# Kernel optimization log

Hardware: AMD Instinct MI355X
Metric: run time of the kernel (lower is better)

## Reference

```python
import jax, jax.numpy as jnp
from jax import lax
import numpy as np

B, C, H, W = 4, 128, 256, 256
HEADS = 8
MID = 256


def conv2d(x, w, stride=1, pad=0, groups=1, mode='zeros'):
    if pad:
        m = 'reflect' if mode == 'reflect' else 'constant'
        x = jnp.pad(x, ((0, 0), (0, 0), (pad, pad), (pad, pad)), mode=m)
    return lax.conv_general_dilated(
        x, w, (stride, stride), 'VALID',
        dimension_numbers=('NCHW', 'OIHW', 'NCHW'),
        feature_group_count=groups)


def layernorm(x, w, b, eps=1e-5):
    # torch LayerNorm over channel dim (applied to b (hw) c layout)
    mu = jnp.mean(x, axis=1, keepdims=True)
    var = jnp.mean((x - mu) ** 2, axis=1, keepdims=True)
    xn = (x - mu) * lax.rsqrt(var + eps)
    return xn * w[None, :, None, None] + b[None, :, None, None]


def l2norm(x, eps=1e-12):
    n = jnp.sqrt(jnp.sum(x * x, axis=-1, keepdims=True))
    return x / jnp.maximum(n, eps)


def setup_inputs() -> dict:
    key = jax.random.key(0)
    ks = jax.random.split(key, 20)
    s = 0.02
    inp = {
        'x': jax.random.normal(ks[0], (B, C, H, W), jnp.float32),
        'illu_feat': jax.random.uniform(ks[1], (B, C, H, W), jnp.float32),
        'ln1_w': jnp.ones((C,), jnp.float32),
        'ln1_b': jnp.zeros((C,), jnp.float32),
        'q_w': jax.random.normal(ks[2], (C, 1, 3, 3), jnp.float32) * s,
        'k_w': jax.random.normal(ks[3], (C, C, 3, 3), jnp.float32) * s,
        'v_w': jax.random.normal(ks[4], (C, C, 1, 1), jnp.float32) * s,
        'a1_w': jax.random.normal(ks[5], (C, 1, 3, 3), jnp.float32) * s,
        'a2_w': jax.random.normal(ks[6], (C // 2, C, 1, 1), jnp.float32) * s,
        'a2_b': jnp.zeros((C // 2,), jnp.float32),
        'temp_a': jnp.ones((HEADS, 1, 1), jnp.float32),
        'temp_v': jnp.ones((HEADS, 1, 1), jnp.float32),
        'po_w': jax.random.normal(ks[7], (C, C, 1, 1), jnp.float32) * s,
        'ln2_w': jnp.ones((C,), jnp.float32),
        'ln2_b': jnp.zeros((C,), jnp.float32),
        'p1_w': jax.random.normal(ks[8], (MID, C, 1, 1), jnp.float32) * s,
        'p1_b': jnp.zeros((MID,), jnp.float32),
        'dw_w': jax.random.normal(ks[9], (MID, 1, 3, 3), jnp.float32) * s,
        'dw_b': jnp.zeros((MID,), jnp.float32),
        'p2_w': jax.random.normal(ks[10], (C, MID, 1, 1), jnp.float32) * s,
        'p2_b': jnp.zeros((C,), jnp.float32),
    }
    return inp


def reference(x, illu_feat, ln1_w, ln1_b, q_w, k_w, v_w, a1_w, a2_w, a2_b,
              temp_a, temp_v, po_w, ln2_w, ln2_b, p1_w, p1_b, dw_w, dw_b,
              p2_w, p2_b):
    b, c, h, w = x.shape
    # ---- Attention branch ----
    xn = layernorm(x, ln1_w, ln1_b)
    q = conv2d(xn, q_w, stride=2, pad=1, groups=c, mode='reflect')  # (b,c,h/2,w/2)
    k = conv2d(xn, k_w, stride=2, pad=1, mode='reflect')            # (b,c,h/2,w/2)
    v = conv2d(xn, v_w) * illu_feat                                 # (b,c,h,w)
    a = conv2d(conv2d(xn, a1_w, stride=2, pad=1, groups=c, mode='reflect'), a2_w)
    a = a + a2_b[None, :, None, None]                               # (b,c/2,h/2,w/2)

    h2, w2 = q.shape[-2:]
    l4 = h2 * w2
    cp = c // HEADS            # channels per head (q,k,v)
    ca = (c // 2) // HEADS     # channels per head (a)
    qr = l2norm(q.reshape(b, HEADS, cp, l4))
    kr = l2norm(k.reshape(b, HEADS, cp, l4))
    ar = l2norm(a.reshape(b, HEADS, ca, l4))
    vr = v.reshape(b, HEADS, cp, h * w)

    attn_a = jax.nn.softmax(jnp.einsum('bhcl,bhdl->bhcd', qr, ar) * temp_a, axis=-1)
    attn_k = jax.nn.softmax(jnp.einsum('bhdl,bhcl->bhdc', ar, kr) * temp_v, axis=-1)
    out_v = jnp.einsum('bhdc,bhcm->bhdm', attn_k, vr)   # (b,h,ca,HW)
    out = jnp.einsum('bhcd,bhdm->bhcm', attn_a, out_v)  # (b,h,cp,HW)
    out = out.reshape(b, c, h, w)
    x = x + conv2d(out, po_w)

    # ---- FFN branch ----
    y = layernorm(x, ln2_w, ln2_b)
    y = conv2d(y, p1_w) + p1_b[None, :, None, None]
    y = conv2d(y, dw_w, pad=1, groups=MID) + dw_b[None, :, None, None]
    y = jax.nn.relu(y)
    y = conv2d(y, p2_w) + p2_b[None, :, None, None]
    return x + y
```

## Files before the change

kernel.cpp:

```cpp
#include <hip/hip_runtime.h>

#define BB 4
#define CC 128
#define HH 256
#define WW 256
#define HWSZ 65536
#define H2 128
#define W2 128
#define L4SZ 16384
#define MIDC 256
#define NHEADS 8

typedef __attribute__((ext_vector_type(8))) short short8;
typedef __attribute__((ext_vector_type(4))) short s16x4;
typedef __attribute__((ext_vector_type(4))) float f32x4;
typedef __attribute__((ext_vector_type(4))) unsigned u32x4;
typedef __attribute__((ext_vector_type(2))) unsigned u32x2;

__device__ __forceinline__ short f2bf(float v) {
  unsigned u = __builtin_bit_cast(unsigned, v);
  u += 0x7fffu + ((u >> 16) & 1u);
  return (short)(u >> 16);
}
__device__ __forceinline__ unsigned pk2(float a, float b) {
  return (unsigned)(unsigned short)f2bf(a) | ((unsigned)(unsigned short)f2bf(b) << 16);
}
__device__ __forceinline__ float bflo(unsigned u) { return __builtin_bit_cast(float, u << 16); }
__device__ __forceinline__ float bfhi(unsigned u) { return __builtin_bit_cast(float, u & 0xffff0000u); }
__device__ __forceinline__ float b2f(short s) {
  return __builtin_bit_cast(float, ((unsigned)(unsigned short)s) << 16);
}

__global__ __launch_bounds__(256) void k_ln1(const float* __restrict__ x,
                                             const float* __restrict__ w,
                                             const float* __restrict__ b,
                                             short* __restrict__ xnt) {
  __shared__ float reds[4][64], red2[4][64];
  __shared__ u32x4 tile[1024];
  int blk = blockIdx.x;
  int bi = blk >> 10, p0 = (blk & 1023) * 64;
  int tid = threadIdx.x, pxl = tid & 63, cs = tid >> 6;
  const float* xp = x + (size_t)(bi * CC + cs * 32) * HWSZ + p0 + pxl;
  float v[32];
  float s = 0.f, s2 = 0.f;
#pragma unroll
  for (int j = 0; j < 32; j++) { float t = xp[j * HWSZ]; v[j] = t; s += t; s2 += t * t; }
  reds[cs][pxl] = s; red2[cs][pxl] = s2;
  __syncthreads();
  float st  = reds[0][pxl] + reds[1][pxl] + reds[2][pxl] + reds[3][pxl];
  float s2t = red2[0][pxl] + red2[1][pxl] + red2[2][pxl] + red2[3][pxl];
  float mu = st * (1.f / CC);
  float rstd = rsqrtf(s2t * (1.f / CC) - mu * mu + 1e-5f);
#pragma unroll
  for (int q = 0; q < 4; q++) {
    u32x4 pk;
#pragma unroll
    for (int e = 0; e < 4; e++) {
      int j = q * 8 + e * 2;
      int c = cs * 32 + j;
      pk[e] = pk2((v[j] - mu) * rstd * w[c] + b[c],
                  (v[j + 1] - mu) * rstd * w[c + 1] + b[c + 1]);
    }
    tile[pxl * 16 + ((cs * 4 + q) ^ (pxl & 7))] = pk;
  }
  __syncthreads();
  u32x4* dst = (u32x4*)xnt + (size_t)(bi * HWSZ + p0) * 16;
  for (int it = 0; it < 4; it++) {
    int f = it * 256 + tid;
    int px = f >> 4, gg = f & 15;
    dst[f] = tile[px * 16 + (gg ^ (px & 7))];
  }
}

__global__ __launch_bounds__(256) void k_wcast(const float* __restrict__ kw,
                                               short* __restrict__ wt) {
  int idx = blockIdx.x * 256 + threadIdx.x;
  if (idx >= 9 * 128 * 128) return;
  int ci = idx & 127, co = (idx >> 7) & 127, tap = idx >> 14;
  wt[idx] = f2bf(kw[(co * CC + ci) * 9 + tap]);
}

__global__ __launch_bounds__(256) void k_prep1(const float* __restrict__ vw,
                                               const float* __restrict__ p1w,
                                               const float* __restrict__ lnw,
                                               const float* __restrict__ lnb,
                                               const float* __restrict__ p1b,
                                               const float* __restrict__ p2w,
                                               const float* __restrict__ qw,
                                               const float* __restrict__ a1w,
                                               const float* __restrict__ dww,
                                               short* __restrict__ vwb,
                                               short* __restrict__ w1p,
                                               short* __restrict__ p2wb,
                                               float* __restrict__ s1,
                                               float* __restrict__ s2f,
                                               float* __restrict__ qwt,
                                               float* __restrict__ a1wt,
                                               float* __restrict__ dwwt) {
  int idx = blockIdx.x * 256 + threadIdx.x;
  if (idx < 16384) vwb[idx] = f2bf(vw[idx]);
  int i2 = idx - 16384;
  if (i2 >= 0 && i2 < 32768) { int c = i2 & 127; w1p[i2] = f2bf(p1w[i2] * lnw[c]); }
  int i3 = idx - 49152;
  if (i3 >= 0 && i3 < 32768) p2wb[i3] = f2bf(p2w[i3]);
  int i4 = idx - 81920;
  if (i4 >= 0 && i4 < 256) {
    float a = 0.f, bb2 = 0.f;
    for (int c = 0; c < 128; c++) {
      a   += p1w[i4 * 128 + c] * lnw[c];
      bb2 += p1w[i4 * 128 + c] * lnb[c];
    }
    s1[i4] = a; s2f[i4] = bb2 + p1b[i4];
  }
  int i5 = idx - 82176;
  if (i5 >= 0 && i5 < 1152) { int tap = i5 >> 7, c = i5 & 127; qwt[i5] = qw[c * 9 + tap]; }
  int i6 = idx - 83328;
  if (i6 >= 0 && i6 < 1152) { int tap = i6 >> 7, c = i6 & 127; a1wt[i6] = a1w[c * 9 + tap]; }
  int i7 = idx - 84480;
  if (i7 >= 0 && i7 < 2304) { int tap = i7 / 256, c = i7 - tap * 256; dwwt[i7] = dww[c * 9 + tap]; }
}

__global__ __launch_bounds__(256) void k_prep2(const float* __restrict__ po,
                                               const float* __restrict__ attnA,
                                               const float* __restrict__ attnK,
                                               short* __restrict__ Mb) {
  __shared__ float T[8][16][16];
  int b = blockIdx.x;
  int tid = threadIdx.x;
  for (int i = tid; i < 2048; i += 256) {
    int h = i >> 8, c = (i >> 4) & 15, cc = i & 15;
    float s = 0.f;
#pragma unroll
    for (int d = 0; d < 8; d++)
      s += attnA[((b * 8 + h) * 16 + c) * 8 + d] * attnK[((b * 8 + h) * 8 + d) * 16 + cc];
    T[h][c][cc] = s;
  }
  __syncthreads();
  for (int i = tid; i < 16384; i += 256) {
    int co = i >> 7, cj = i & 127, h = cj >> 4, cc = cj & 15;
    float s = 0.f;
#pragma unroll
    for (int c = 0; c < 16; c++) s += po[co * 128 + h * 16 + c] * T[h][c][cc];
    Mb[b * 16384 + i] = f2bf(s);
  }
}

__global__ __launch_bounds__(256) void k_dwsn(const short* __restrict__ xnt,
                                              const float* __restrict__ qwt,
                                              const float* __restrict__ a1wt,
                                              short* __restrict__ qg,
                                              short* __restrict__ a1g) {
  int blk = blockIdx.x;
  int xg = blk & 1, y = (blk >> 1) & 127, b = blk >> 8;
  int oct = threadIdx.x & 15, pxq = threadIdx.x >> 4;
  int x0 = xg * 64 + pxq * 4;
  float aq[4][8], aa[4][8];
#pragma unroll
  for (int j = 0; j < 4; j++)
#pragma unroll
    for (int c = 0; c < 8; c++) { aq[j][c] = 0.f; aa[j][c] = 0.f; }
#pragma unroll
  for (int tap = 0; tap < 9; tap++) {
    int dy = tap / 3, dx = tap - 3 * dy;
    int ry = 2 * y + dy - 1; ry = ry < 0 ? -ry : ry;
    float4 wq0 = *(const float4*)(qwt + tap * 128 + oct * 8);
    float4 wq1 = *(const float4*)(qwt + tap * 128 + oct * 8 + 4);
    float4 wa0 = *(const float4*)(a1wt + tap * 128 + oct * 8);
    float4 wa1 = *(const float4*)(a1wt + tap * 128 + oct * 8 + 4);
#pragma unroll
    for (int jq = 0; jq < 4; jq++) {
      int ix = 2 * (x0 + jq) + dx - 1; ix = ix < 0 ? -ix : ix;
      short8 xv = *(const short8*)(xnt + (size_t)((b * HWSZ + ry * WW + ix) * CC) + oct * 8);
      float f0 = b2f(xv[0]), f1 = b2f(xv[1]), f2 = b2f(xv[2]), f3 = b2f(xv[3]);
      float f4 = b2f(xv[4]), f5 = b2f(xv[5]), f6 = b2f(xv[6]), f7 = b2f(xv[7]);
      aq[jq][0] += wq0.x * f0; aq[jq][1] += wq0.y * f1; aq[jq][2] += wq0.z * f2; aq[jq][3] += wq0.w * f3;
      aq[jq][4] += wq1.x * f4; aq[jq][5] += wq1.y * f5; aq[jq][6] += wq1.z * f6; aq[jq][7] += wq1.w * f7;
      aa[jq][0] += wa0.x * f0; aa[jq][1] += wa0.y * f1; aa[jq][2] += wa0.z * f2; aa[jq][3] += wa0.w * f3;
      aa[jq][4] += wa1.x * f4; aa[jq][5] += wa1.y * f5; aa[jq][6] += wa1.z * f6; aa[jq][7] += wa1.w * f7;
    }
  }
  int pb = y * 128 + x0;
#pragma unroll
  for (int j = 0; j < 8; j++) {
    s16x4 vq = { f2bf(aq[0][j]), f2bf(aq[1][j]), f2bf(aq[2][j]), f2bf(aq[3][j]) };
    s16x4 va = { f2bf(aa[0][j]), f2bf(aa[1][j]), f2bf(aa[2][j]), f2bf(aa[3][j]) };
    *(s16x4*)(qg  + (size_t)(b * CC + oct * 8 + j) * L4SZ + pb) = vq;
    *(s16x4*)(a1g + (size_t)(b * CC + oct * 8 + j) * L4SZ + pb) = va;
  }
}

__global__ __launch_bounds__(256) void k_kconv_mfma(const short* __restrict__ xnt,
                                                    const short* __restrict__ wt,
                                                    short* __restrict__ kg) {
  __shared__ short8 ldsb[1156];
  int blk = blockIdx.x;
  int bx = blk & 15, by = (blk >> 4) & 15, bi = blk >> 8;
  int r0 = by * 16 - 1, c0 = bx * 16 - 1;
  int lane = threadIdx.x & 63, wv = threadIdx.x >> 6;
  int px0 = wv * 16;
  int pxl = px0 + (lane & 15);
  int py = pxl >> 3, pxx = pxl & 7;
  int g = lane >> 4;
  f32x4 acc[8];
#pragma unroll
  for (int m = 0; m < 8; m++) acc[m] = (f32x4){0.f, 0.f, 0.f, 0.f};
  for (int ci0 = 0; ci0 < CC; ci0 += 32) {
    __syncthreads();
    for (int i = threadIdx.x; i < 1156; i += 256) {
      int p = i >> 2, gg = i & 3;
      int rr = p / 17, cc = p - rr * 17;
      int gr = r0 + rr; gr = gr < 0 ? -gr : gr;
      int gc = c0 + cc; gc = gc < 0 ? -gc : gc;
      int slot = gg ^ ((p >> 1) & 3);
      ldsb[p * 4 + slot] =
          *(const short8*)(xnt + (size_t)((bi * HWSZ + gr * WW + gc) * CC + ci0 + gg * 8));
    }
    __syncthreads();
#pragma unroll
    for (int tap = 0; tap < 9; tap++) {
      int dy = tap / 3, dx = tap - dy * 3;
      int p = (2 * py + dy) * 17 + 2 * pxx + dx;
      int slot = g ^ ((p >> 1) & 3);
      short8 bfrag = ldsb[p * 4 + slot];
      const short* wbase = wt + (tap * 128 + (lane & 15)) * 128 + ci0 + g * 8;
#pragma unroll
      for (int m = 0; m < 8; m++) {
        short8 afrag = *(const short8*)(wbase + m * 16 * 128);
        acc[m] = __builtin_amdgcn_mfma_f32_16x16x32_bf16(afrag, bfrag, acc[m], 0, 0, 0);
      }
    }
  }
  int oy = by * 8 + py, ox = bx * 8 + pxx;
  int rb = g * 4;
#pragma unroll
  for (int m = 0; m < 8; m++)
#pragma unroll
    for (int r = 0; r < 4; r++)
      kg[(size_t)(bi * CC + m * 16 + rb + r) * L4SZ + oy * W2 + ox] = f2bf(acc[m][r]);
}

__global__ __launch_bounds__(256) void k_a2(const short* __restrict__ a1g,
                                            const float* __restrict__ w,
                                            const float* __restrict__ bias,
                                            short* __restrict__ ab) {
  __shared__ float t[CC][64];
  int blk = blockIdx.x;
  int bi = blk >> 8;
  int p0 = (blk & 255) * 64;
  for (int i = threadIdx.x; i < CC * 64; i += 256) {
    int ci = i >> 6, px = i & 63;
    t[ci][px] = b2f(a1g[(size_t)(bi * CC + ci) * L4SZ + p0 + px]);
  }
  __syncthreads();
  int px = threadIdx.x & 63;
  int co0 = ((__builtin_amdgcn_readfirstlane((int)threadIdx.x)) >> 6) << 4;
  float acc[16];
#pragma unroll
  for (int j = 0; j < 16; j++) acc[j] = 0.f;
  for (int ci = 0; ci < CC; ci++) {
    float in = t[ci][px];
#pragma unroll
    for (int j = 0; j < 16; j++) acc[j] += w[(co0 + j) * CC + ci] * in;
  }
#pragma unroll
  for (int j = 0; j < 16; j++)
    ab[(size_t)(bi * 64 + co0 + j) * L4SZ + p0 + px] = f2bf(acc[j] + bias[co0 + j]);
}

__global__ __launch_bounds__(256) void k_gram(const short* __restrict__ qg,
                                              const short* __restrict__ kg,
                                              const short* __restrict__ ag,
                                              float* __restrict__ partial) {
  __shared__ float red[4][1280];
  int blk = blockIdx.x;
  int bh = blk >> 3, chunk = blk & 7;
  int b = bh >> 3, h = bh & 7;
  int tid = threadIdx.x, lane = tid & 63, wv = tid >> 6;
  int cl = lane & 15, g = lane >> 4;
  const short* qb = qg + (size_t)(b * 128 + h * 16 + cl) * L4SZ;
  const short* kb = kg + (size_t)(b * 128 + h * 16 + cl) * L4SZ;
  const short* ar = ag + (size_t)(b * 64 + h * 8 + cl) * L4SZ;
  int k0 = chunk * 2048 + wv * 512 + g * 8;
  f32x4 t0 = {0,0,0,0}, t1 = {0,0,0,0}, t2 = {0,0,0,0}, t3 = {0,0,0,0}, t4 = {0,0,0,0};
#pragma unroll 4
  for (int ks = 0; ks < 16; ks++) {
    int ko = k0 + ks * 32;
    short8 fq = *(const short8*)(qb + ko);
    short8 fk = *(const short8*)(kb + ko);
    short8 fa = *(const short8*)(ar + ko);
    t0 = __builtin_amdgcn_mfma_f32_16x16x32_bf16(fq, fa, t0, 0, 0, 0);
    t1 = __builtin_amdgcn_mfma_f32_16x16x32_bf16(fa, fk, t1, 0, 0, 0);
    t2 = __builtin_amdgcn_mfma_f32_16x16x32_bf16(fq, fq, t2, 0, 0, 0);
    t3 = __builtin_amdgcn_mfma_f32_16x16x32_bf16(fk, fk, t3, 0, 0, 0);
    t4 = __builtin_amdgcn_mfma_f32_16x16x32_bf16(fa, fa, t4, 0, 0, 0);
  }
#pragma unroll
  for (int r = 0; r < 4; r++) {
    int flat = (g * 4 + r) * 16 + cl;
    red[wv][flat]        = t0[r];
    red[wv][256 + flat]  = t1[r];
    red[wv][512 + flat]  = t2[r];
    red[wv][768 + flat]  = t3[r];
    red[wv][1024 + flat] = t4[r];
  }
  __syncthreads();
  float* po = partial + (size_t)(bh * 8 + chunk) * 1280;
  for (int i = tid; i < 1280; i += 256)
    po[i] = red[0][i] + red[1][i] + red[2][i] + red[3][i];
}

__global__ __launch_bounds__(64) void k_softmax2(const float* __restrict__ partial,
                                                 const float* __restrict__ tA,
                                                 const float* __restrict__ tV,
                                                 float* __restrict__ attnA,
                                                 float* __restrict__ attnK) {
  __shared__ float S[1280];
  int bh = blockIdx.x;
  int h = bh & 7;
  for (int i = threadIdx.x; i < 1280; i += 64) {
    float s = 0.f;
    for (int c = 0; c < 8; c++) s += partial[(size_t)(bh * 8 + c) * 1280 + i];
    S[i] = s;
  }
  __syncthreads();
  float ta = tA[h], tv = tV[h];
  if (threadIdx.x < 16) {
    int c = threadIdx.x;
    float nq = fmaxf(sqrtf(S[512 + c * 17]), 1e-12f);
    float lg[8]; float m = -1e30f;
#pragma unroll
    for (int e = 0; e < 8; e++) {
      float na = fmaxf(sqrtf(S[1024 + e * 17]), 1e-12f);
      lg[e] = S[c * 16 + e] / (nq * na) * ta;
      m = fmaxf(m, lg[e]);
    }
    float sum = 0.f;
#pragma unroll
    for (int e = 0; e < 8; e++) { lg[e] = expf(lg[e] - m); sum += lg[e]; }
    float inv = 1.f / sum;
#pragma unroll
    for (int e = 0; e < 8; e++) attnA[(bh * 16 + c) * 8 + e] = lg[e] * inv;
  } else if (threadIdx.x < 24) {
    int e = threadIdx.x - 16;
    float na = fmaxf(sqrtf(S[1024 + e * 17]), 1e-12f);
    float lg[16]; float m = -1e30f;
#pragma unroll
    for (int c = 0; c < 16; c++) {
      float nk = fmaxf(sqrtf(S[768 + c * 17]), 1e-12f);
      lg[c] = S[256 + e * 16 + c] / (na * nk) * tv;
      m = fmaxf(m, lg[c]);
    }
    float sum = 0.f;
#pragma unroll
    for (int c = 0; c < 16; c++) { lg[c] = expf(lg[c] - m); sum += lg[c]; }
    float inv = 1.f / sum;
#pragma unroll
    for (int c = 0; c < 16; c++) attnK[(bh * 8 + e) * 16 + c] = lg[c] * inv;
  }
}

__global__ __launch_bounds__(256) void k_vx2(const short* __restrict__ xnt,
                                             const float* __restrict__ illu,
                                             const float* __restrict__ x,
                                             const short* __restrict__ vwb,
                                             const short* __restrict__ Mb,
                                             u32x4* __restrict__ x2n4,
                                             float* __restrict__ mu,
                                             float* __restrict__ rs) {
  __shared__ unsigned lds[4608];
  int blk = blockIdx.x;
  int bi = blk >> 10, p0 = (blk & 1023) * 64;
  int tid = threadIdx.x, lane = tid & 63, wv = tid >> 6;
  int cl = lane & 15, g = lane >> 4;
  int px = wv * 16 + cl;
  float ilv[32];
#pragma unroll
  for (int m = 0; m < 8; m++)
#pragma unroll
    for (int r = 0; r < 4; r++)
      ilv[m * 4 + r] = illu[(size_t)(bi * CC + m * 16 + g * 4 + r) * HWSZ + p0 + px];
  const u32x4* xsrc = (const u32x4*)(xnt + ((size_t)(bi * HWSZ + p0) << 7));
  for (int it = 0; it < 4; it++) {
    int idx = it * 256 + tid;
    int pp = idx >> 4, gg = idx & 15;
    u32x4 v = xsrc[pp * 16 + gg];
    ((u32x4*)lds)[pp * 16 + (gg ^ (pp & 7))] = v;
  }
  __syncthreads();
  f32x4 acc[8];
#pragma unroll
  for (int m = 0; m < 8; m++) acc[m] = (f32x4){0.f, 0.f, 0.f, 0.f};
#pragma unroll
  for (int kc = 0; kc < 4; kc++) {
    short8 bf = *(const short8*)((const short*)lds + px * 128 + (((kc * 4 + g) ^ (px & 7)) * 8));
#pragma unroll
    for (int m = 0; m < 8; m++) {
      short8 af = *(const short8*)(vwb + (m * 16 + cl) * 128 + kc * 32 + g * 8);
      acc[m] = __builtin_amdgcn_mfma_f32_16x16x32_bf16(af, bf, acc[m], 0, 0, 0);
    }
  }
  __syncthreads();
#pragma unroll
  for (int m = 0; m < 8; m++) {
    float v0 = acc[m][0] * ilv[m * 4 + 0];
    float v1 = acc[m][1] * ilv[m * 4 + 1];
    float v2 = acc[m][2] * ilv[m * 4 + 2];
    float v3 = acc[m][3] * ilv[m * 4 + 3];
    int gi = 2 * m + (g >> 1);
    unsigned* dst = lds + px * 64 + ((gi ^ (px & 7)) << 2) + (g & 1) * 2;
    dst[0] = pk2(v0, v1);
    dst[1] = pk2(v2, v3);
  }
  __syncthreads();
  float xv[32];
#pragma unroll
  for (int m = 0; m < 8; m++)
#pragma unroll
    for (int r = 0; r < 4; r++)
      xv[m * 4 + r] = x[(size_t)(bi * CC + m * 16 + g * 4 + r) * HWSZ + p0 + px];
  f32x4 acc2[8];
#pragma unroll
  for (int m = 0; m < 8; m++) acc2[m] = (f32x4){0.f, 0.f, 0.f, 0.f};
  const short* Mbb = Mb + bi * 16384;
#pragma unroll
  for (int kc = 0; kc < 4; kc++) {
    short8 bf = *(const short8*)((const short*)lds + px * 128 + (((kc * 4 + g) ^ (px & 7)) * 8));
#pragma unroll
    for (int m = 0; m < 8; m++) {
      short8 af = *(const short8*)(Mbb + (m * 16 + cl) * 128 + kc * 32 + g * 8);
      acc2[m] = __builtin_amdgcn_mfma_f32_16x16x32_bf16(af, bf, acc2[m], 0, 0, 0);
    }
  }
  float s = 0.f, s2 = 0.f;
  unsigned xp[16];
#pragma unroll
  for (int m = 0; m < 8; m++) {
    float tv[4];
#pragma unroll
    for (int r = 0; r < 4; r++) {
      float t = xv[m * 4 + r] + acc2[m][r];
      tv[r] = t; s += t; s2 += t * t;
    }
    xp[2 * m]     = pk2(tv[0], tv[1]);
    xp[2 * m + 1] = pk2(tv[2], tv[3]);
  }
  s  += __shfl_xor(s, 16);  s  += __shfl_xor(s, 32);
  s2 += __shfl_xor(s2, 16); s2 += __shfl_xor(s2, 32);
  float muv = s * (1.f / 128.f);
  float rsv = rsqrtf(s2 * (1.f / 128.f) - muv * muv + 1e-5f);
  if (g == 0) { mu[bi * HWSZ + p0 + px] = muv; rs[bi * HWSZ + p0 + px] = rsv; }
  __syncthreads();
#pragma unroll
  for (int m = 0; m < 8; m++) {
    lds[px * 68 + m * 8 + g * 2 + 0] = xp[2 * m];
    lds[px * 68 + m * 8 + g * 2 + 1] = xp[2 * m + 1];
  }
  __syncthreads();
  u32x4* dst4 = x2n4 + (size_t)(bi * HWSZ + p0) * 16;
  for (int it = 0; it < 4; it++) {
    int flat = it * 256 + tid;
    int pp = flat >> 4, j = flat & 15;
    dst4[flat] = *(const u32x4*)(lds + pp * 68 + j * 4);
  }
}

__global__ __launch_bounds__(256) void k_p1(const u32x4* __restrict__ x2n4,
                                            const short* __restrict__ w1p,
                                            const float* __restrict__ s1,
                                            const float* __restrict__ s2f,
                                            const float* __restrict__ mu,
                                            const float* __restrict__ rs,
                                            u32x4* __restrict__ y1g) {
  __shared__ u32x4 bt[1024];
  __shared__ u32x4 olds[2048];
  int blk = blockIdx.x;
  int bi = blk >> 10, p0 = (blk & 1023) * 64;
  int tid = threadIdx.x, lane = tid & 63, wv = tid >> 6;
  int cl = lane & 15, g = lane >> 4;
  for (int f = tid; f < 1024; f += 256) {
    int px = f >> 4, kg = f & 15;
    bt[kg * 64 + (px ^ kg)] = x2n4[(size_t)(bi * HWSZ + p0 + px) * 16 + kg];
  }
  __syncthreads();
  f32x4 acc[4][4];
#pragma unroll
  for (int mt = 0; mt < 4; mt++)
#pragma unroll
    for (int n = 0; n < 4; n++) acc[mt][n] = (f32x4){0.f, 0.f, 0.f, 0.f};
#pragma unroll
  for (int kc = 0; kc < 4; kc++) {
    short8 bfr[4];
#pragma unroll
    for (int n = 0; n < 4; n++) {
      int px = n * 16 + cl, kgi = kc * 4 + g;
      bfr[n] = __builtin_bit_cast(short8, bt[kgi * 64 + (px ^ kgi)]);
    }
#pragma unroll
    for (int mt = 0; mt < 4; mt++) {
      short8 af = *(const short8*)(w1p + (wv * 64 + mt * 16 + cl) * 128 + kc * 32 + g * 8);
#pragma unroll
      for (int n = 0; n < 4; n++)
        acc[mt][n] = __builtin_amdgcn_mfma_f32_16x16x32_bf16(af, bfr[n], acc[mt][n], 0, 0, 0);
    }
  }
  float muv[4], rsv[4];
#pragma unroll
  for (int n = 0; n < 4; n++) {
    muv[n] = mu[bi * HWSZ + p0 + n * 16 + cl];
    rsv[n] = rs[bi * HWSZ + p0 + n * 16 + cl];
  }
#pragma unroll
  for (int mt = 0; mt < 4; mt++) {
    int mid = wv * 64 + mt * 16 + g * 4;
    float4 s1v = *(const float4*)(s1 + mid);
    float4 s2v = *(const float4*)(s2f + mid);
    int gi = wv * 8 + mt * 2 + (g >> 1);
#pragma unroll
    for (int n = 0; n < 4; n++) {
      int px = n * 16 + cl;
      float y0 = rsv[n] * (acc[mt][n][0] - muv[n] * s1v.x) + s2v.x;
      float y1 = rsv[n] * (acc[mt][n][1] - muv[n] * s1v.y) + s2v.y;
      float y2 = rsv[n] * (acc[mt][n][2] - muv[n] * s1v.z) + s2v.z;
      float y3 = rsv[n] * (acc[mt][n][3] - muv[n] * s1v.w) + s2v.w;
      unsigned* dp = (unsigned*)&olds[gi * 64 + px] + (g & 1) * 2;
      dp[0] = pk2(y0, y1);
      dp[1] = pk2(y2, y3);
    }
  }
  __syncthreads();
  for (int it = 0; it < 8; it++) {
    int f = it * 256 + tid;
    int gi = f >> 6, px = f & 63;
    y1g[(size_t)gi * (BB * HWSZ) + bi * HWSZ + p0 + px] = olds[gi * 64 + px];
  }
}

__global__ __launch_bounds__(256) void k_ffn2(const u32x4* __restrict__ y1g,
                                              const float* __restrict__ dwwt,
                                              const float* __restrict__ dwb,
                                              const short* __restrict__ p2wb,
                                              const float* __restrict__ p2b,
                                              const u32x4* __restrict__ x2n4,
                                              float* __restrict__ out) {
  __shared__ u32x4 ylds[1600];
  __shared__ u32x4 dwt[1024];
  int blk = blockIdx.x;
  int tx = blk & 31, ty = (blk >> 5) & 31, b = blk >> 10;
  int r0 = ty * 8 - 1, c0 = tx * 8 - 1;
  int tid = threadIdx.x, lane = tid & 63, wv = tid >> 6;
  int cl = lane & 15, g = lane >> 4;
  int pp = tid & 63;
  int qy = pp >> 3, qx = pp & 7;
  f32x4 acc[2][4];
#pragma unroll
  for (int mt = 0; mt < 2; mt++)
#pragma unroll
    for (int n = 0; n < 4; n++) acc[mt][n] = (f32x4){0.f, 0.f, 0.f, 0.f};
  for (int ch = 0; ch < 2; ch++) {
    if (ch) __syncthreads();
    for (int i = tid; i < 1600; i += 256) {
      int gg = i / 100, p = i - gg * 100;
      int rr = p / 10, cc = p - rr * 10;
      int gr = r0 + rr, gc = c0 + cc;
      u32x4 v = (u32x4){0u, 0u, 0u, 0u};
      if (gr >= 0 && gr < HH && gc >= 0 && gc < WW)
        v = y1g[(size_t)(ch * 16 + gg) * (BB * HWSZ) + b * HWSZ + gr * WW + gc];
      ylds[gg * 100 + p] = v;
    }
    __syncthreads();
#pragma unroll
    for (int e = 0; e < 4; e++) {
      int gran = wv * 4 + e;
      float sdw[8];
#pragma unroll
      for (int j = 0; j < 8; j++) sdw[j] = 0.f;
#pragma unroll
      for (int tap = 0; tap < 9; tap++) {
        int dy = tap / 3, dx = tap - 3 * dy;
        int p = (qy + dy) * 10 + qx + dx;
        u32x4 vv = ylds[gran * 100 + p];
        const float* wp = dwwt + tap * 256 + ch * 128 + gran * 8;
        sdw[0] += wp[0] * bflo(vv.x);
        sdw[1] += wp[1] * bfhi(vv.x);
        sdw[2] += wp[2] * bflo(vv.y);
        sdw[3] += wp[3] * bfhi(vv.y);
        sdw[4] += wp[4] * bflo(vv.z);
        sdw[5] += wp[5] * bfhi(vv.z);
        sdw[6] += wp[6] * bflo(vv.w);
        sdw[7] += wp[7] * bfhi(vv.w);
      }
      const float* db = dwb + ch * 128 + gran * 8;
      u32x4 pkv;
      pkv.x = pk2(fmaxf(sdw[0] + db[0], 0.f), fmaxf(sdw[1] + db[1], 0.f));
      pkv.y = pk2(fmaxf(sdw[2] + db[2], 0.f), fmaxf(sdw[3] + db[3], 0.f));
      pkv.z = pk2(fmaxf(sdw[4] + db[4], 0.f), fmaxf(sdw[5] + db[5], 0.f));
      pkv.w = pk2(fmaxf(sdw[6] + db[6], 0.f), fmaxf(sdw[7] + db[7], 0.f));
      dwt[gran * 64 + pp] = pkv;
    }
    __syncthreads();
#pragma unroll
    for (int kc = 0; kc < 4; kc++) {
      short8 af0 = *(const short8*)(p2wb + (wv * 32 + cl) * 256 + ch * 128 + kc * 32 + g * 8);
      short8 af1 = *(const short8*)(p2wb + (wv * 32 + 16 + cl) * 256 + ch * 128 + kc * 32 + g * 8);
      int gi = kc * 4 + g;
#pragma unroll
      for (int n = 0; n < 4; n++) {
        int px = n * 16 + cl;
        short8 bf = __builtin_bit_cast(short8, dwt[gi * 64 + px]);
        acc[0][n] = __builtin_amdgcn_mfma_f32_16x16x32_bf16(af0, bf, acc[0][n], 0, 0, 0);
        acc[1][n] = __builtin_amdgcn_mfma_f32_16x16x32_bf16(af1, bf, acc[1][n], 0, 0, 0);
      }
    }
  }
  __syncthreads();
  for (int f = tid; f < 1024; f += 256) {
    int pxa = f >> 4, gg = f & 15;
    u32x4 v = x2n4[(size_t)(b * HWSZ + (ty * 8 + (pxa >> 3)) * WW + tx * 8 + (pxa & 7)) * 16 + gg];
    ylds[gg * 64 + (pxa ^ (gg & 7))] = v;
  }
  __syncthreads();
#pragma unroll
  for (int mt = 0; mt < 2; mt++) {
    int cob = wv * 32 + mt * 16 + g * 4;
    int q = cob >> 3;
    float pb0 = p2b[cob + 0], pb1 = p2b[cob + 1], pb2 = p2b[cob + 2], pb3 = p2b[cob + 3];
#pragma unroll
    for (int n = 0; n < 4; n++) {
      int px = n * 16 + cl;
      const unsigned* xr = (const unsigned*)&ylds[q * 64 + (px ^ (q & 7))] + (g & 1) * 2;
      unsigned xa = xr[0], xb2 = xr[1];
      int oy = ty * 8 + (px >> 3), ox = tx * 8 + (px & 7);
      size_t gi = (size_t)(b * CC + cob) * HWSZ + oy * WW + ox;
      out[gi]             = bflo(xa)  + acc[mt][n][0] + pb0;
      out[gi + HWSZ]      = bfhi(xa)  + acc[mt][n][1] + pb1;
      out[gi + 2 * HWSZ]  = bflo(xb2) + acc[mt][n][2] + pb2;
      out[gi + 3 * HWSZ]  = bfhi(xb2) + acc[mt][n][3] + pb3;
    }
  }
}

extern "C" void kernel_launch(void* const* d_in, const int* in_sizes, int n_in,
                              void* d_out, int out_size, void* d_ws, size_t ws_size,
                              hipStream_t stream) {
  const float* x    = (const float*)d_in[0];
  const float* illu = (const float*)d_in[1];
  const float* ln1w = (const float*)d_in[2];
  const float* ln1b = (const float*)d_in[3];
  const float* qw   = (const float*)d_in[4];
  const float* kw   = (const float*)d_in[5];
  const float* vw   = (const float*)d_in[6];
  const float* a1w  = (const float*)d_in[7];
  const float* a2w  = (const float*)d_in[8];
  const float* a2b  = (const float*)d_in[9];
  const float* tA   = (const float*)d_in[10];
  const float* tV   = (const float*)d_in[11];
  const float* pow_ = (const float*)d_in[12];
  const float* ln2w = (const float*)d_in[13];
  const float* ln2b = (const float*)d_in[14];
  const float* p1w  = (const float*)d_in[15];
  const float* p1b  = (const float*)d_in[16];
  const float* dww  = (const float*)d_in[17];
  const float* dwb  = (const float*)d_in[18];
  const float* p2w  = (const float*)d_in[19];
  const float* p2b  = (const float*)d_in[20];
  float* out = (float*)d_out;

  float* ws    = (float*)d_ws;
  u32x4* x2n4  = (u32x4*)ws;
  float* mu    = ws + 16777216;
  float* rs    = ws + 17039360;
  float* attnA = ws + 17301504;
  float* attnK = ws + 17305600;
  short* vwb   = (short*)(ws + 17309696);
  short* w1p   = (short*)(ws + 17317888);
  short* p2wb  = (short*)(ws + 17334272);
  short* Mb    = (short*)(ws + 17350656);
  float* s1    = ws + 17383424;
  float* s2f   = ws + 17383680;
  short* wt    = (short*)(ws + 17383936);
  float* qwt   = ws + 17457664;
  float* a1wt  = ws + 17458816;
  float* dwwt  = ws + 17459968;
  u32x4* y1g   = (u32x4*)(ws + 17462272);
  short* xnt   = (short*)(ws + 17462272);
  short* qg    = (short*)(ws + 34239488);
  short* kgb   = (short*)(ws + 38433792);
  short* a1g   = (short*)(ws + 42628096);
  short* ab    = (short*)(ws + 46822400);
  float* partial = ws + 48919552;

  k_ln1<<<4096, 256, 0, stream>>>(x, ln1w, ln1b, xnt);
  k_wcast<<<576, 256, 0, stream>>>(kw, wt);
  k_prep1<<<340, 256, 0, stream>>>(vw, p1w, ln2w, ln2b, p1b, p2w, qw, a1w, dww,
                                   vwb, w1p, p2wb, s1, s2f, qwt, a1wt, dwwt);
  k_dwsn<<<1024, 256, 0, stream>>>(xnt, qwt, a1wt, qg, a1g);
  k_kconv_mfma<<<1024, 256, 0, stream>>>(xnt, wt, kgb);
  k_a2<<<1024, 256, 0, stream>>>(a1g, a2w, a2b, ab);
  k_gram<<<256, 256, 0, stream>>>(qg, kgb, ab, partial);
  k_softmax2<<<32, 64, 0, stream>>>(partial, tA, tV, attnA, attnK);
  k_prep2<<<4, 256, 0, stream>>>(pow_, attnA, attnK, Mb);
  k_vx2<<<4096, 256, 0, stream>>>(xnt, illu, x, vwb, Mb, x2n4, mu, rs);
  k_p1<<<4096, 256, 0, stream>>>(x2n4, w1p, s1, s2f, mu, rs, y1g);
  k_ffn2<<<4096, 256, 0, stream>>>(y1g, dwwt, dwb, p2wb, p2b, x2n4, out);
}
```

Measured before the change: 769.5 us.

## Store FFN mid activations pixel-major and read depthwise taps directly from global

```diff
diff --git a/kernel.cpp b/kernel.cpp
--- a/kernel.cpp
+++ b/kernel.cpp
@@ -470,7 +470,7 @@
                                             const float* __restrict__ s2f,
                                             const float* __restrict__ mu,
                                             const float* __restrict__ rs,
-                                            u32x4* __restrict__ y1g) {
+                                            u32x4* __restrict__ y1n4) {
   __shared__ u32x4 bt[1024];
   __shared__ u32x4 olds[2048];
   int blk = blockIdx.x;
@@ -522,34 +522,34 @@
       float y1 = rsv[n] * (acc[mt][n][1] - muv[n] * s1v.y) + s2v.y;
       float y2 = rsv[n] * (acc[mt][n][2] - muv[n] * s1v.z) + s2v.z;
       float y3 = rsv[n] * (acc[mt][n][3] - muv[n] * s1v.w) + s2v.w;
-      unsigned* dp = (unsigned*)&olds[gi * 64 + px] + (g & 1) * 2;
+      unsigned* dp = (unsigned*)&olds[px * 32 + (gi ^ (px & 7))] + (g & 1) * 2;
       dp[0] = pk2(y0, y1);
       dp[1] = pk2(y2, y3);
     }
   }
   __syncthreads();
+  u32x4* dst = y1n4 + (size_t)(bi * HWSZ + p0) * 32;
   for (int it = 0; it < 8; it++) {
     int f = it * 256 + tid;
-    int gi = f >> 6, px = f & 63;
-    y1g[(size_t)gi * (BB * HWSZ) + bi * HWSZ + p0 + px] = olds[gi * 64 + px];
-  }
-}
-
-__global__ __launch_bounds__(256) void k_ffn2(const u32x4* __restrict__ y1g,
+    int px = f >> 5, gi = f & 31;
+    dst[f] = olds[px * 32 + (gi ^ (px & 7))];
+  }
+}
+
+__global__ __launch_bounds__(256) void k_dwp2(const u32x4* __restrict__ y1n4,
                                               const float* __restrict__ dwwt,
                                               const float* __restrict__ dwb,
                                               const short* __restrict__ p2wb,
                                               const float* __restrict__ p2b,
                                               const u32x4* __restrict__ x2n4,
                                               float* __restrict__ out) {
-  __shared__ u32x4 ylds[1600];
   __shared__ u32x4 dwt[1024];
   int blk = blockIdx.x;
   int tx = blk & 31, ty = (blk >> 5) & 31, b = blk >> 10;
   int r0 = ty * 8 - 1, c0 = tx * 8 - 1;
   int tid = threadIdx.x, lane = tid & 63, wv = tid >> 6;
   int cl = lane & 15, g = lane >> 4;
-  int pp = tid & 63;
+  int pp = tid & 63, grp = tid >> 6;
   int qy = pp >> 3, qx = pp & 7;
   f32x4 acc[2][4];
 #pragma unroll
@@ -557,45 +557,46 @@
 #pragma unroll
     for (int n = 0; n < 4; n++) acc[mt][n] = (f32x4){0.f, 0.f, 0.f, 0.f};
   for (int ch = 0; ch < 2; ch++) {
+    float sdw[32];
+#pragma unroll
+    for (int j = 0; j < 32; j++) sdw[j] = 0.f;
+#pragma unroll
+    for (int tap = 0; tap < 9; tap++) {
+      int dy = tap / 3, dx = tap - 3 * dy;
+      int gr = r0 + qy + dy, gc = c0 + qx + dx;
+      u32x4 v0 = {0,0,0,0}, v1 = {0,0,0,0}, v2 = {0,0,0,0}, v3 = {0,0,0,0};
+      if (gr >= 0 && gr < HH && gc >= 0 && gc < WW) {
+        const u32x4* src = y1n4 + (size_t)(b * HWSZ + gr * WW + gc) * 32 + ch * 16 + grp * 4;
+        v0 = src[0]; v1 = src[1]; v2 = src[2]; v3 = src[3];
+      }
+      const float* wp = dwwt + tap * 256 + ch * 128 + grp * 32;
+      sdw[0]  += wp[0]  * bflo(v0.x); sdw[1]  += wp[1]  * bfhi(v0.x);
+      sdw[2]  += wp[2]  * bflo(v0.y); sdw[3]  += wp[3]  * bfhi(v0.y);
+      sdw[4]  += wp[4]  * bflo(v0.z); sdw[5]  += wp[5]  * bfhi(v0.z);
+      sdw[6]  += wp[6]  * bflo(v0.w); sdw[7]  += wp[7]  * bfhi(v0.w);
+      sdw[8]  += wp[8]  * bflo(v1.x); sdw[9]  += wp[9]  * bfhi(v1.x);
+      sdw[10] += wp[10] * bflo(v1.y); sdw[11] += wp[11] * bfhi(v1.y);
+      sdw[12] += wp[12] * bflo(v1.z); sdw[13] += wp[13] * bfhi(v1.z);
+      sdw[14] += wp[14] * bflo(v1.w); sdw[15] += wp[15] * bfhi(v1.w);
+      sdw[16] += wp[16] * bflo(v2.x); sdw[17] += wp[17] * bfhi(v2.x);
+      sdw[18] += wp[18] * bflo(v2.y); sdw[19] += wp[19] * bfhi(v2.y);
+      sdw[20] += wp[20] * bflo(v2.z); sdw[21] += wp[21] * bfhi(v2.z);
+      sdw[22] += wp[22] * bflo(v2.w); sdw[23] += wp[23] * bfhi(v2.w);
+      sdw[24] += wp[24] * bflo(v3.x); sdw[25] += wp[25] * bfhi(v3.x);
+      sdw[26] += wp[26] * bflo(v3.y); sdw[27] += wp[27] * bfhi(v3.y);
+      sdw[28] += wp[28] * bflo(v3.z); sdw[29] += wp[29] * bfhi(v3.z);
+      sdw[30] += wp[30] * bflo(v3.w); sdw[31] += wp[31] * bfhi(v3.w);
+    }
     if (ch) __syncthreads();
-    for (int i = tid; i < 1600; i += 256) {
-      int gg = i / 100, p = i - gg * 100;
-      int rr = p / 10, cc = p - rr * 10;
-      int gr = r0 + rr, gc = c0 + cc;
-      u32x4 v = (u32x4){0u, 0u, 0u, 0u};
-      if (gr >= 0 && gr < HH && gc >= 0 && gc < WW)
-        v = y1g[(size_t)(ch * 16 + gg) * (BB * HWSZ) + b * HWSZ + gr * WW + gc];
-      ylds[gg * 100 + p] = v;
-    }
-    __syncthreads();
+    const float* db = dwb + ch * 128 + grp * 32;
 #pragma unroll
     for (int e = 0; e < 4; e++) {
-      int gran = wv * 4 + e;
-      float sdw[8];
-#pragma unroll
-      for (int j = 0; j < 8; j++) sdw[j] = 0.f;
-#pragma unroll
-      for (int tap = 0; tap < 9; tap++) {
-        int dy = tap / 3, dx = tap - 3 * dy;
-        int p = (qy + dy) * 10 + qx + dx;
-        u32x4 vv = ylds[gran * 100 + p];
-        const float* wp = dwwt + tap * 256 + ch * 128 + gran * 8;
-        sdw[0] += wp[0] * bflo(vv.x);
-        sdw[1] += wp[1] * bfhi(vv.x);
-        sdw[2] += wp[2] * bflo(vv.y);
-        sdw[3] += wp[3] * bfhi(vv.y);
-        sdw[4] += wp[4] * bflo(vv.z);
-        sdw[5] += wp[5] * bfhi(vv.z);
-        sdw[6] += wp[6] * bflo(vv.w);
-        sdw[7] += wp[7] * bfhi(vv.w);
-      }
-      const float* db = dwb + ch * 128 + gran * 8;
       u32x4 pkv;
-      pkv.x = pk2(fmaxf(sdw[0] + db[0], 0.f), fmaxf(sdw[1] + db[1], 0.f));
-      pkv.y = pk2(fmaxf(sdw[2] + db[2], 0.f), fmaxf(sdw[3] + db[3], 0.f));
-      pkv.z = pk2(fmaxf(sdw[4] + db[4], 0.f), fmaxf(sdw[5] + db[5], 0.f));
-      pkv.w = pk2(fmaxf(sdw[6] + db[6], 0.f), fmaxf(sdw[7] + db[7], 0.f));
-      dwt[gran * 64 + pp] = pkv;
+      pkv.x = pk2(fmaxf(sdw[e * 8 + 0] + db[e * 8 + 0], 0.f), fmaxf(sdw[e * 8 + 1] + db[e * 8 + 1], 0.f));
+      pkv.y = pk2(fmaxf(sdw[e * 8 + 2] + db[e * 8 + 2], 0.f), fmaxf(sdw[e * 8 + 3] + db[e * 8 + 3], 0.f));
+      pkv.z = pk2(fmaxf(sdw[e * 8 + 4] + db[e * 8 + 4], 0.f), fmaxf(sdw[e * 8 + 5] + db[e * 8 + 5], 0.f));
+      pkv.w = pk2(fmaxf(sdw[e * 8 + 6] + db[e * 8 + 6], 0.f), fmaxf(sdw[e * 8 + 7] + db[e * 8 + 7], 0.f));
+      dwt[(grp * 4 + e) * 64 + pp] = pkv;
     }
     __syncthreads();
 #pragma unroll
@@ -616,7 +617,7 @@
   for (int f = tid; f < 1024; f += 256) {
     int pxa = f >> 4, gg = f & 15;
     u32x4 v = x2n4[(size_t)(b * HWSZ + (ty * 8 + (pxa >> 3)) * WW + tx * 8 + (pxa & 7)) * 16 + gg];
-    ylds[gg * 64 + (pxa ^ (gg & 7))] = v;
+    dwt[gg * 64 + (pxa ^ (gg & 7))] = v;
   }
   __syncthreads();
 #pragma unroll
@@ -627,7 +628,7 @@
 #pragma unroll
     for (int n = 0; n < 4; n++) {
       int px = n * 16 + cl;
-      const unsigned* xr = (const unsigned*)&ylds[q * 64 + (px ^ (q & 7))] + (g & 1) * 2;
+      const unsigned* xr = (const unsigned*)&dwt[q * 64 + (px ^ (q & 7))] + (g & 1) * 2;
       unsigned xa = xr[0], xb2 = xr[1];
       int oy = ty * 8 + (px >> 3), ox = tx * 8 + (px & 7);
       size_t gi = (size_t)(b * CC + cob) * HWSZ + oy * WW + ox;
@@ -681,7 +682,7 @@
   float* qwt   = ws + 17457664;
   float* a1wt  = ws + 17458816;
   float* dwwt  = ws + 17459968;
-  u32x4* y1g   = (u32x4*)(ws + 17462272);
+  u32x4* y1n4  = (u32x4*)(ws + 17462272);
   short* xnt   = (short*)(ws + 17462272);
   short* qg    = (short*)(ws + 34239488);
   short* kgb   = (short*)(ws + 38433792);
@@ -700,6 +701,6 @@
   k_softmax2<<<32, 64, 0, stream>>>(partial, tA, tV, attnA, attnK);
   k_prep2<<<4, 256, 0, stream>>>(pow_, attnA, attnK, Mb);
   k_vx2<<<4096, 256, 0, stream>>>(xnt, illu, x, vwb, Mb, x2n4, mu, rs);
-  k_p1<<<4096, 256, 0, stream>>>(x2n4, w1p, s1, s2f, mu, rs, y1g);
-  k_ffn2<<<4096, 256, 0, stream>>>(y1g, dwwt, dwb, p2wb, p2b, x2n4, out);
-}
+  k_p1<<<4096, 256, 0, stream>>>(x2n4, w1p, s1, s2f, mu, rs, y1n4);
+  k_dwp2<<<4096, 256, 0, stream>>>(y1n4, dwwt, dwb, p2wb, p2b, x2n4, out);
+}
```

Result: slower. 877.0 us (+14.0%).
